# Optimization experiments

Hardware: AMD Instinct MI355X
Metric: run time of the kernel (lower is better)

Reference implementation:

```python
import jax, jax.numpy as jnp
import numpy as np

B, K = 2048, 256
ED = RD = HD = 256
AD = ED + RD          # action_dim = 512
IN = ED + HD + RD     # 768
NUM_E, NUM_R = 100000, 500
HUGE = jnp.float32(1e31)  # ops.HUGE_INT


def setup_inputs() -> dict:
    key = jax.random.key(0)
    ks = jax.random.split(key, 12)
    s = 0.05  # keep logits in a sane range
    E = jax.random.normal(ks[0], (B, ED), jnp.float32)
    H = jax.random.normal(ks[1], (B, HD), jnp.float32)
    Q = jax.random.normal(ks[2], (B, RD), jnp.float32)
    W1 = jax.random.normal(ks[3], (AD, IN), jnp.float32) * s
    b1 = jnp.zeros((AD,), jnp.float32)
    W2 = jax.random.normal(ks[4], (AD, AD), jnp.float32) * s
    b2 = jnp.zeros((AD,), jnp.float32)
    emb_r = jax.random.normal(ks[5], (NUM_R, RD), jnp.float32) * s
    emb_e = jax.random.normal(ks[6], (NUM_E, ED), jnp.float32) * s
    # binary action mask (variable-size action spaces, padded); col 0 always valid
    action_mask = (jax.random.uniform(ks[7], (B, K)) > 0.3).astype(jnp.float32)
    action_mask = action_mask.at[:, 0].set(1.0)
    r_space = jax.random.randint(ks[8], (B, K), 0, NUM_R)
    e_space = jax.random.randint(ks[9], (B, K), 0, NUM_E)
    return {"E": E, "H": H, "Q": Q, "W1": W1, "b1": b1, "W2": W2, "b2": b2,
            "emb_r": emb_r, "emb_e": emb_e, "action_mask": action_mask,
            "r_space": r_space, "e_space": e_space}


def reference(E, H, Q, W1, b1, W2, b2, emb_r, emb_e, action_mask, r_space, e_space):
    # state MLP: X = W2Dropout(W2(relu(W1(cat([E, H, Q])))))  (dropout = identity at eval)
    X = jnp.concatenate([E, H, Q], axis=-1)           # [B, IN]
    X = jax.nn.relu(X @ W1.T + b1)                    # [B, AD]
    X2 = X @ W2.T + b2                                # [B, AD]
    # gather action embeddings: A = cat([emb_r[r], emb_e[e]])  [B, K, AD]
    A = jnp.concatenate([emb_r[r_space], emb_e[e_space]], axis=-1)
    # masked softmax over action space
    scores = jnp.einsum('bkd,bd->bk', A, X2) - (1.0 - action_mask) * HUGE
    action_dist = jax.nn.softmax(scores, axis=-1)     # [B, K]
    entropy = -jnp.sum(action_dist * jnp.log(action_dist + 1e-20), axis=-1)  # [B]
    return action_dist, entropy
```

## Files before the change

kernel.cpp:

```cpp
#include <hip/hip_runtime.h>
#include <hip/hip_bf16.h>
#include <hip/hip_fp8.h>
#include <math.h>

#define B_   2048
#define K_   256
#define AD_  512
#define IN_  768
#define NR_  500
#define NRP_ 512
#define NE_  100000
#define PITCH 72

typedef __attribute__((ext_vector_type(8))) short short8;
typedef __attribute__((ext_vector_type(4))) float float4v;
typedef __attribute__((ext_vector_type(4))) float f32x4;

__device__ __forceinline__ unsigned short f2bf(float f) {
    unsigned int u = __float_as_uint(f);
    unsigned int r = u + 0x7FFF + ((u >> 16) & 1);
    return (unsigned short)(r >> 16);
}
__device__ __forceinline__ unsigned char f2fp8(float f) {
    __hip_fp8_e4m3 t(f);
    return (unsigned char)t.__x;
}
__device__ __forceinline__ float fp8tof(unsigned int byte) {
    __hip_fp8_e4m3 t; t.__x = (__hip_fp8_storage_t)byte; return (float)t;
}
__device__ __forceinline__ float dot4_fp8(unsigned int d, const float* x) {
    return fp8tof(d & 0xffu)         * x[0] + fp8tof((d >> 8) & 0xffu)  * x[1]
         + fp8tof((d >> 16) & 0xffu) * x[2] + fp8tof(d >> 24)           * x[3];
}
__device__ __forceinline__ short8 pack8(float4 a, float4 b) {
    short8 r;
    r[0] = (short)f2bf(a.x); r[1] = (short)f2bf(a.y);
    r[2] = (short)f2bf(a.z); r[3] = (short)f2bf(a.w);
    r[4] = (short)f2bf(b.x); r[5] = (short)f2bf(b.y);
    r[6] = (short)f2bf(b.z); r[7] = (short)f2bf(b.w);
    return r;
}

#define EE_N4 (NE_ * 256 / 4)
__device__ __forceinline__ void conv_range(
    const float* __restrict__ emb_e, unsigned char* __restrict__ emb_e8,
    int q0, int q1, int cb, int nb)
{
    const int stride = nb * 256;
    const f32x4* __restrict__ src = (const f32x4*)emb_e;
    uchar4* __restrict__ dst = (uchar4*)emb_e8;
    int i = q0 + cb * 256 + (int)threadIdx.x;
    for (; i + 3 * stride < q1; i += 4 * stride) {
        f32x4 v0 = __builtin_nontemporal_load(src + i);
        f32x4 v1 = __builtin_nontemporal_load(src + i + stride);
        f32x4 v2 = __builtin_nontemporal_load(src + i + 2 * stride);
        f32x4 v3 = __builtin_nontemporal_load(src + i + 3 * stride);
        uchar4 o0, o1, o2, o3;
        o0.x = f2fp8(v0[0]); o0.y = f2fp8(v0[1]); o0.z = f2fp8(v0[2]); o0.w = f2fp8(v0[3]);
        o1.x = f2fp8(v1[0]); o1.y = f2fp8(v1[1]); o1.z = f2fp8(v1[2]); o1.w = f2fp8(v1[3]);
        o2.x = f2fp8(v2[0]); o2.y = f2fp8(v2[1]); o2.z = f2fp8(v2[2]); o2.w = f2fp8(v2[3]);
        o3.x = f2fp8(v3[0]); o3.y = f2fp8(v3[1]); o3.z = f2fp8(v3[2]); o3.w = f2fp8(v3[3]);
        dst[i] = o0; dst[i + stride] = o1; dst[i + 2 * stride] = o2; dst[i + 3 * stride] = o3;
    }
    for (; i < q1; i += stride) {
        f32x4 v = __builtin_nontemporal_load(src + i);
        uchar4 o;
        o.x = f2fp8(v[0]); o.y = f2fp8(v[1]); o.z = f2fp8(v[2]); o.w = f2fp8(v[3]);
        dst[i] = o;
    }
}

__device__ __forceinline__ void br_compute(
    const float* __restrict__ emb_r, const float* __restrict__ b2,
    float* __restrict__ br, int blk)
{
    const int tid = threadIdx.x;
    const int rl = tid >> 3, sub = tid & 7;
    const int r = blk * 32 + rl;
    float acc = 0.0f;
    if (r < NR_) {
        const float4* er = (const float4*)&emb_r[(size_t)r * 256];
        const float4* bb = (const float4*)b2;
        #pragma unroll
        for (int i = 0; i < 8; ++i) {
            const float4 e = er[sub * 8 + i];
            const float4 c = bb[sub * 8 + i];
            acc += e.x * c.x + e.y * c.y + e.z * c.z + e.w * c.w;
        }
    }
    #pragma unroll
    for (int off = 4; off >= 1; off >>= 1) acc += __shfl_down(acc, off, 8);
    if (sub == 0) br[r] = (r < NR_) ? acc : 0.0f;
}

__device__ __forceinline__ void mfma_step(
    const ushort* __restrict__ Asb, const ushort* __restrict__ Bsb,
    int w, int q, int l16, float4v acc[4])
{
    #pragma unroll
    for (int kh = 0; kh < 64; kh += 32) {
        const short8 af = *(const short8*)&Asb[(w * 16 + l16) * PITCH + kh + q * 8];
        #pragma unroll
        for (int jn = 0; jn < 4; ++jn) {
            const short8 bfr = *(const short8*)&Bsb[(jn * 16 + l16) * PITCH + kh + q * 8];
            acc[jn] = __builtin_amdgcn_mfma_f32_16x16x32_bf16(af, bfr, acc[jn], 0, 0, 0);
        }
    }
}

__device__ __forceinline__ const float* ehq_ptr(
    const float* E, const float* H, const float* Q, int m, int k)
{
    return (k < 256) ? &E[(size_t)m * 256 + k]
         : (k < 512) ? &H[(size_t)m * 256 + (k - 256)]
                     : &Q[(size_t)m * 256 + (k - 512)];
}
__device__ __forceinline__ void ld_w2t(const float* __restrict__ W2, int col, int krow,
                                       short8& lo, short8& hi)
{
    float v[16];
    #pragma unroll
    for (int i = 0; i < 16; ++i) v[i] = W2[(size_t)(krow + i) * 512 + col];
    #pragma unroll
    for (int i = 0; i < 8; ++i) { lo[i] = (short)f2bf(v[i]); hi[i] = (short)f2bf(v[8 + i]); }
}
__device__ __forceinline__ void ld_embr(const float* __restrict__ emb_r, int row, int k,
                                        bool ok, short8& lo, short8& hi)
{
    if (ok) {
        const float4* p = (const float4*)&emb_r[(size_t)row * 256 + k];
        lo = pack8(p[0], p[1]); hi = pack8(p[2], p[3]);
    } else {
        #pragma unroll
        for (int i = 0; i < 8; ++i) { lo[i] = 0; hi[i] = 0; }
    }
}

__global__ __launch_bounds__(256) void k1_kernel(
    const float* __restrict__ E, const float* __restrict__ H,
    const float* __restrict__ Q, const float* __restrict__ W1,
    const float* __restrict__ b1, const float* __restrict__ emb_r,
    const float* __restrict__ b2, const float* __restrict__ W2,
    ushort* __restrict__ H1b, ushort* __restrict__ W2Rb, float* __restrict__ br,
    const float* __restrict__ emb_e, unsigned char* __restrict__ emb_e8,
    int q0, int q1, int nbconv)
{
    __shared__ ushort Asl[2][64 * PITCH];
    __shared__ ushort Bsl[2][64 * PITCH];
    const int tid = threadIdx.x;
    const int lane = tid & 63, w = tid >> 6;
    const int q = lane >> 4, l16 = lane & 15;
    const int lrow = tid >> 2, lcg = (tid & 3) * 16;

    if (blockIdx.x >= 8) {
        const int c = (int)(blockIdx.x - 8) * 32 + (int)blockIdx.y;
        if (c >= 80) { conv_range(emb_e, emb_e8, q0, q1, c - 80, nbconv); return; }
        if (c >= 64) { br_compute(emb_r, b2, br, c - 64); return; }
        const int n0 = (c & 7) * 64, m0 = (c >> 3) * 64;
        const int am = m0 + lrow;
        const bool aok = am < NR_;
        short8 pa0, pa1, pb0, pb1;
        ld_embr(emb_r, am, lcg, aok, pa0, pa1);
        ld_w2t(W2, n0 + lrow, lcg, pb0, pb1);
        *(short8*)&Asl[0][lrow * PITCH + lcg]     = pa0;
        *(short8*)&Asl[0][lrow * PITCH + lcg + 8] = pa1;
        *(short8*)&Bsl[0][lrow * PITCH + lcg]     = pb0;
        *(short8*)&Bsl[0][lrow * PITCH + lcg + 8] = pb1;
        float4v acc[4] = {};
        int buf = 0;
        __syncthreads();
        for (int k0 = 0; k0 < 256; k0 += 64) {
            if (k0 + 64 < 256) {
                ld_embr(emb_r, am, k0 + 64 + lcg, aok, pa0, pa1);
                ld_w2t(W2, n0 + lrow, k0 + 64 + lcg, pb0, pb1);
            }
            mfma_step(&Asl[buf][0], &Bsl[buf][0], w, q, l16, acc);
            if (k0 + 64 < 256) {
                *(short8*)&Asl[buf ^ 1][lrow * PITCH + lcg]     = pa0;
                *(short8*)&Asl[buf ^ 1][lrow * PITCH + lcg + 8] = pa1;
                *(short8*)&Bsl[buf ^ 1][lrow * PITCH + lcg]     = pb0;
                *(short8*)&Bsl[buf ^ 1][lrow * PITCH + lcg + 8] = pb1;
                __syncthreads();
                buf ^= 1;
            }
        }
        #pragma unroll
        for (int jn = 0; jn < 4; ++jn) {
            const int n = n0 + jn * 16 + l16;
            #pragma unroll
            for (int r = 0; r < 4; ++r) {
                const int m = m0 + w * 16 + q * 4 + r;
                W2Rb[(size_t)m * 512 + n] = f2bf(acc[jn][r]);
            }
        }
        return;
    }

    const int n0 = blockIdx.x * 64, m0 = blockIdx.y * 64;
    const int am = m0 + lrow;
    const float* w1p = &W1[(size_t)(n0 + lrow) * 768 + lcg];

    short8 pa0, pa1, pb0, pb1;
    {
        const float4* ap = (const float4*)ehq_ptr(E, H, Q, am, lcg);
        pa0 = pack8(ap[0], ap[1]); pa1 = pack8(ap[2], ap[3]);
        const float4* bp = (const float4*)w1p;
        pb0 = pack8(bp[0], bp[1]); pb1 = pack8(bp[2], bp[3]);
    }
    *(short8*)&Asl[0][lrow * PITCH + lcg]     = pa0;
    *(short8*)&Asl[0][lrow * PITCH + lcg + 8] = pa1;
    *(short8*)&Bsl[0][lrow * PITCH + lcg]     = pb0;
    *(short8*)&Bsl[0][lrow * PITCH + lcg + 8] = pb1;
    float4v acc[4] = {};
    int buf = 0;
    __syncthreads();
    for (int k0 = 0; k0 < 768; k0 += 64) {
        if (k0 + 64 < 768) {
            const float4* ap = (const float4*)ehq_ptr(E, H, Q, am, k0 + 64 + lcg);
            pa0 = pack8(ap[0], ap[1]); pa1 = pack8(ap[2], ap[3]);
            const float4* bp = (const float4*)(w1p + k0 + 64);
            pb0 = pack8(bp[0], bp[1]); pb1 = pack8(bp[2], bp[3]);
        }
        mfma_step(&Asl[buf][0], &Bsl[buf][0], w, q, l16, acc);
        if (k0 + 64 < 768) {
            *(short8*)&Asl[buf ^ 1][lrow * PITCH + lcg]     = pa0;
            *(short8*)&Asl[buf ^ 1][lrow * PITCH + lcg + 8] = pa1;
            *(short8*)&Bsl[buf ^ 1][lrow * PITCH + lcg]     = pb0;
            *(short8*)&Bsl[buf ^ 1][lrow * PITCH + lcg + 8] = pb1;
            __syncthreads();
            buf ^= 1;
        }
    }
    #pragma unroll
    for (int jn = 0; jn < 4; ++jn) {
        const int n = n0 + jn * 16 + l16;
        const float bn = b1[n];
        #pragma unroll
        for (int r = 0; r < 4; ++r) {
            const int m = m0 + w * 16 + q * 4 + r;
            H1b[(size_t)m * AD_ + n] = f2bf(fmaxf(acc[jn][r] + bn, 0.0f));
        }
    }
}

__global__ __launch_bounds__(256) void k2_kernel(
    const ushort* __restrict__ H1b, const float* __restrict__ W2,
    const ushort* __restrict__ W2Rb, const float* __restrict__ b2,
    const float* __restrict__ br, float* __restrict__ X2e, float* __restrict__ Rt,
    const float* __restrict__ emb_e, unsigned char* __restrict__ emb_e8,
    int q0, int q1, int nbconv)
{
    __shared__ ushort Asl[2][64 * PITCH];
    __shared__ ushort Bsl[2][64 * PITCH];
    if (blockIdx.x >= 12) {
        conv_range(emb_e, emb_e8, q0, q1,
                   (int)(blockIdx.x - 12) * 32 + (int)blockIdx.y, nbconv);
        return;
    }
    const int tid = threadIdx.x;
    const int lane = tid & 63, w = tid >> 6;
    const int q = lane >> 4, l16 = lane & 15;
    const int lrow = tid >> 2, lcg = (tid & 3) * 16;
    const bool isR = blockIdx.x >= 4;
    const int n0 = isR ? (int)(blockIdx.x - 4) * 64 : (int)blockIdx.x * 64;
    const int m0 = blockIdx.y * 64;

    const ushort* aptr  = &H1b[(size_t)(m0 + lrow) * 512 + lcg];
    const ushort* bptrR = &W2Rb[(size_t)(n0 + lrow) * 512 + lcg];
    const float*  bptrW = &W2[(size_t)(256 + n0 + lrow) * 512 + lcg];

    short8 pa0, pa1, pb0, pb1;
    pa0 = *(const short8*)aptr; pa1 = *(const short8*)(aptr + 8);
    if (isR) { pb0 = *(const short8*)bptrR; pb1 = *(const short8*)(bptrR + 8); }
    else {
        const float4* bp = (const float4*)bptrW;
        pb0 = pack8(bp[0], bp[1]); pb1 = pack8(bp[2], bp[3]);
    }
    *(short8*)&Asl[0][lrow * PITCH + lcg]     = pa0;
    *(short8*)&Asl[0][lrow * PITCH + lcg + 8] = pa1;
    *(short8*)&Bsl[0][lrow * PITCH + lcg]     = pb0;
    *(short8*)&Bsl[0][lrow * PITCH + lcg + 8] = pb1;
    float4v acc[4] = {};
    int buf = 0;
    __syncthreads();
    for (int k0 = 0; k0 < 512; k0 += 64) {
        if (k0 + 64 < 512) {
            pa0 = *(const short8*)(aptr + k0 + 64);
            pa1 = *(const short8*)(aptr + k0 + 64 + 8);
            if (isR) {
                pb0 = *(const short8*)(bptrR + k0 + 64);
                pb1 = *(const short8*)(bptrR + k0 + 64 + 8);
            } else {
                const float4* bp = (const float4*)(bptrW + k0 + 64);
                pb0 = pack8(bp[0], bp[1]); pb1 = pack8(bp[2], bp[3]);
            }
        }
        mfma_step(&Asl[buf][0], &Bsl[buf][0], w, q, l16, acc);
        if (k0 + 64 < 512) {
            *(short8*)&Asl[buf ^ 1][lrow * PITCH + lcg]     = pa0;
            *(short8*)&Asl[buf ^ 1][lrow * PITCH + lcg + 8] = pa1;
            *(short8*)&Bsl[buf ^ 1][lrow * PITCH + lcg]     = pb0;
            *(short8*)&Bsl[buf ^ 1][lrow * PITCH + lcg + 8] = pb1;
            __syncthreads();
            buf ^= 1;
        }
    }
    #pragma unroll
    for (int jn = 0; jn < 4; ++jn) {
        const int n = n0 + jn * 16 + l16;
        const float bn = isR ? br[n] : b2[256 + n];
        #pragma unroll
        for (int r = 0; r < 4; ++r) {
            const int m = m0 + w * 16 + q * 4 + r;
            const float cv = acc[jn][r] + bn;
            if (isR) Rt[(size_t)m * 512 + n] = cv;
            else     X2e[(size_t)m * 256 + n] = cv;
        }
    }
}

__global__ __launch_bounds__(256) void scores_kernel(
    const float* __restrict__ X2e, const float* __restrict__ R,
    const unsigned char* __restrict__ emb_e8, const float* __restrict__ mask,
    const int* __restrict__ r_space, const int* __restrict__ e_space,
    float* __restrict__ dist, float* __restrict__ entropy)
{
    const int b = blockIdx.x;
    const int tid = threadIdx.x;
    const int lane = tid & 63, wid = tid >> 6;
    const int l16 = lane & 15, q4 = lane >> 4;

    __shared__ int   s_e[K_];
    __shared__ float s_dot[K_];
    __shared__ float s_red[12];

    const int   e_mine = e_space[b * K_ + tid];
    const int   r_mine = r_space[b * K_ + tid];
    const float mk     = mask[b * K_ + tid];
    s_e[tid] = (mk != 0.0f) ? e_mine : 0;
    const float bias   = R[(size_t)b * NRP_ + r_mine] - (1.0f - mk) * 1e31f;
    float x[16];
    #pragma unroll
    for (int i = 0; i < 4; ++i) {
        const float4 xv = *(const float4*)&X2e[(size_t)b * 256 + l16 * 16 + i * 4];
        x[i * 4 + 0] = xv.x; x[i * 4 + 1] = xv.y;
        x[i * 4 + 2] = xv.z; x[i * 4 + 3] = xv.w;
    }
    __syncthreads();

    const int kbase = wid * 64;
    #pragma unroll
    for (int it = 0; it < 2; ++it) {
        uint4 wv[8];
        #pragma unroll
        for (int u = 0; u < 8; ++u) {
            const int row = kbase + it * 32 + u * 4 + q4;
            const int e = s_e[row];
            wv[u] = *(const uint4*)&emb_e8[(size_t)e * 256 + l16 * 16];
        }
        float p[8];
        #pragma unroll
        for (int u = 0; u < 8; ++u) {
            p[u] = dot4_fp8(wv[u].x, &x[0]) + dot4_fp8(wv[u].y, &x[4])
                 + dot4_fp8(wv[u].z, &x[8]) + dot4_fp8(wv[u].w, &x[12]);
        }
        #pragma unroll
        for (int off = 8; off >= 1; off >>= 1) {
            #pragma unroll
            for (int u = 0; u < 8; ++u) p[u] += __shfl_down(p[u], off, 16);
        }
        if (l16 == 0) {
            #pragma unroll
            for (int u = 0; u < 8; ++u) s_dot[kbase + it * 32 + u * 4 + q4] = p[u];
        }
    }
    __syncthreads();

    const float v = s_dot[tid] + bias;

    float m = v;
    #pragma unroll
    for (int off = 32; off >= 1; off >>= 1) m = fmaxf(m, __shfl_down(m, off));
    if (lane == 0) s_red[wid] = m;
    __syncthreads();
    if (tid == 0)
        s_red[8] = fmaxf(fmaxf(s_red[0], s_red[1]), fmaxf(s_red[2], s_red[3]));
    __syncthreads();
    const float bmax = s_red[8];

    const float ev = __expf(v - bmax);
    float s = ev;
    float t = ev * (v - bmax);
    #pragma unroll
    for (int off = 32; off >= 1; off >>= 1) {
        s += __shfl_down(s, off);
        t += __shfl_down(t, off);
    }
    if (lane == 0) { s_red[wid] = s; s_red[4 + wid] = t; }
    __syncthreads();
    if (tid == 0) {
        s_red[9]  = s_red[0] + s_red[1] + s_red[2] + s_red[3];
        s_red[10] = s_red[4] + s_red[5] + s_red[6] + s_red[7];
    }
    __syncthreads();
    const float ssum = s_red[9];

    dist[(size_t)b * K_ + tid] = ev / ssum;
    if (tid == 0)
        entropy[b] = logf(ssum) - s_red[10] / ssum;
}

extern "C" void kernel_launch(void* const* d_in, const int* in_sizes, int n_in,
                              void* d_out, int out_size, void* d_ws, size_t ws_size,
                              hipStream_t stream) {
    const float* E     = (const float*)d_in[0];
    const float* H     = (const float*)d_in[1];
    const float* Q     = (const float*)d_in[2];
    const float* W1    = (const float*)d_in[3];
    const float* b1    = (const float*)d_in[4];
    const float* W2    = (const float*)d_in[5];
    const float* b2    = (const float*)d_in[6];
    const float* emb_r = (const float*)d_in[7];
    const float* emb_e = (const float*)d_in[8];
    const float* mask  = (const float*)d_in[9];
    const int* r_space = (const int*)d_in[10];
    const int* e_space = (const int*)d_in[11];

    float* out_dist = (float*)d_out;
    float* out_ent  = out_dist + (size_t)B_ * K_;

    char* ws = (char*)d_ws;
    unsigned char* emb_e8 = (unsigned char*)ws; ws += (size_t)NE_ * 256;
    ushort* H1b  = (ushort*)ws;  ws += (size_t)B_ * AD_ * 2;
    ushort* W2Rb = (ushort*)ws;  ws += (size_t)512 * 512 * 2;
    float*  X2e  = (float*)ws;   ws += (size_t)B_ * 256 * 4;
    float*  Rt   = (float*)ws;   ws += (size_t)B_ * NRP_ * 4;
    float*  br   = (float*)ws;   ws += (size_t)NRP_ * 4;

    const int Q1V = 3712000;

    dim3 g(16, 32);
    k1_kernel<<<g, 256, 0, stream>>>(E, H, Q, W1, b1, emb_r, b2, W2,
                                     H1b, W2Rb, br, emb_e, emb_e8, 0, Q1V, 176);
    k2_kernel<<<g, 256, 0, stream>>>(H1b, W2, W2Rb, b2, br, X2e, Rt,
                                     emb_e, emb_e8, Q1V, EE_N4, 128);
    scores_kernel<<<B_, 256, 0, stream>>>(X2e, Rt, emb_e8, mask,
                                          r_space, e_space, out_dist, out_ent);
}
```

Baseline: 214.6 us.

## Pre-convert GEMM inputs to bf16 in a prep kernel and widen score gather batch

Adds a prep kernel that converts the concatenated E/H/Q input, W1 and the entity half of W2 to bf16 once. The two GEMM kernels then load bf16 tiles directly through a shared templated tile routine, which removes the fp32 loads and per-tile packing inside the MFMA loops. The scores kernel now issues all 16 gathered emb_e8 row loads per thread at once instead of two batches of 8, to expose more memory-level parallelism. The cost is an extra kernel launch, an extra round trip of the small tensors through memory, and higher register use in the scores kernel.

```diff
diff --git a/kernel.cpp b/kernel.cpp
--- a/kernel.cpp
+++ b/kernel.cpp
@@ -39,6 +39,39 @@
     r[4] = (short)f2bf(b.x); r[5] = (short)f2bf(b.y);
     r[6] = (short)f2bf(b.z); r[7] = (short)f2bf(b.w);
     return r;
+}
+
+#define X_N4   (B_ * IN_ / 4)
+#define W1_N4  (AD_ * IN_ / 4)
+#define W2E_N4 (256 * AD_ / 4)
+#define PREPS_TOTAL (X_N4 + W1_N4 + W2E_N4)
+__global__ __launch_bounds__(256) void prep_small_kernel(
+    const float* __restrict__ E, const float* __restrict__ H,
+    const float* __restrict__ Q, const float* __restrict__ W1,
+    const float* __restrict__ W2,
+    ushort* __restrict__ Xb, ushort* __restrict__ W1b, ushort* __restrict__ W2eb)
+{
+    int t = blockIdx.x * 256 + threadIdx.x;
+    const float* src; ushort* dst; int off;
+    if (t < X_N4) {
+        const int base = t * 4;
+        const int row = base / IN_, col = base % IN_;
+        src = (col < 256) ? &E[row * 256 + col]
+            : (col < 512) ? &H[row * 256 + col - 256]
+                          : &Q[row * 256 + col - 512];
+        const float4 v = *(const float4*)src;
+        ushort4 o;
+        o.x = f2bf(v.x); o.y = f2bf(v.y); o.z = f2bf(v.z); o.w = f2bf(v.w);
+        *(ushort4*)&Xb[base] = o;
+        return;
+    }
+    t -= X_N4;
+    if (t < W1_N4) { src = W1;                dst = W1b;  off = t; }
+    else           { src = W2 + 256 * AD_;    dst = W2eb; off = t - W1_N4; }
+    const float4 v = *(const float4*)&src[off * 4];
+    ushort4 o;
+    o.x = f2bf(v.x); o.y = f2bf(v.y); o.z = f2bf(v.z); o.w = f2bf(v.w);
+    *(ushort4*)&dst[off * 4] = o;
 }
 
 #define EE_N4 (NE_ * 256 / 4)
@@ -90,7 +123,7 @@
     }
     #pragma unroll
     for (int off = 4; off >= 1; off >>= 1) acc += __shfl_down(acc, off, 8);
-    if (sub == 0) br[r] = (r < NR_) ? acc : 0.0f;
+    if (sub == 0 && r < NRP_) br[r] = (r < NR_) ? acc : 0.0f;
 }
 
 __device__ __forceinline__ void mfma_step(
@@ -108,13 +141,66 @@
     }
 }
 
-__device__ __forceinline__ const float* ehq_ptr(
-    const float* E, const float* H, const float* Q, int m, int k)
-{
-    return (k < 256) ? &E[(size_t)m * 256 + k]
-         : (k < 512) ? &H[(size_t)m * 256 + (k - 256)]
-                     : &Q[(size_t)m * 256 + (k - 512)];
-}
+template<int K, bool RELU, bool OUT_BF16>
+__device__ __forceinline__ void gemm_tile(
+    const ushort* __restrict__ A, const ushort* __restrict__ Bw,
+    const float* __restrict__ bias, ushort* __restrict__ outb,
+    float* __restrict__ outf, const int ostride,
+    const int n0, const int m0, ushort* __restrict__ As, ushort* __restrict__ Bs)
+{
+    const int tid = threadIdx.x;
+    const int lane = tid & 63, w = tid >> 6;
+    const int lrow = tid >> 2, lcg = (tid & 3) * 16;
+    const int q = lane >> 4, l16 = lane & 15;
+
+    const ushort* aptr = &A[(size_t)(m0 + lrow) * K + lcg];
+    const ushort* bptr = &Bw[(size_t)(n0 + lrow) * K + lcg];
+
+    short8 ra0 = *(const short8*)aptr;
+    short8 ra1 = *(const short8*)(aptr + 8);
+    short8 rb0 = *(const short8*)bptr;
+    short8 rb1 = *(const short8*)(bptr + 8);
+    *(short8*)&As[lrow * PITCH + lcg]     = ra0;
+    *(short8*)&As[lrow * PITCH + lcg + 8] = ra1;
+    *(short8*)&Bs[lrow * PITCH + lcg]     = rb0;
+    *(short8*)&Bs[lrow * PITCH + lcg + 8] = rb1;
+
+    float4v acc[4] = {};
+    int buf = 0;
+    __syncthreads();
+    for (int k0 = 0; k0 < K; k0 += 64) {
+        if (k0 + 64 < K) {
+            ra0 = *(const short8*)(aptr + k0 + 64);
+            ra1 = *(const short8*)(aptr + k0 + 64 + 8);
+            rb0 = *(const short8*)(bptr + k0 + 64);
+            rb1 = *(const short8*)(bptr + k0 + 64 + 8);
+        }
+        mfma_step(As + buf * 64 * PITCH, Bs + buf * 64 * PITCH, w, q, l16, acc);
+        if (k0 + 64 < K) {
+            const int nb = (buf ^ 1) * 64 * PITCH;
+            *(short8*)&As[nb + lrow * PITCH + lcg]     = ra0;
+            *(short8*)&As[nb + lrow * PITCH + lcg + 8] = ra1;
+            *(short8*)&Bs[nb + lrow * PITCH + lcg]     = rb0;
+            *(short8*)&Bs[nb + lrow * PITCH + lcg + 8] = rb1;
+            __syncthreads();
+            buf ^= 1;
+        }
+    }
+    #pragma unroll
+    for (int jn = 0; jn < 4; ++jn) {
+        const int n = n0 + jn * 16 + l16;
+        const float bn = bias[n];
+        #pragma unroll
+        for (int r = 0; r < 4; ++r) {
+            const int m = m0 + w * 16 + q * 4 + r;
+            float c = acc[jn][r] + bn;
+            if (RELU) c = fmaxf(c, 0.0f);
+            if (OUT_BF16) outb[(size_t)m * ostride + n] = f2bf(c);
+            else          outf[(size_t)m * ostride + n] = c;
+        }
+    }
+}
+
 __device__ __forceinline__ void ld_w2t(const float* __restrict__ W2, int col, int krow,
                                        short8& lo, short8& hi)
 {
@@ -135,187 +221,99 @@
         for (int i = 0; i < 8; ++i) { lo[i] = 0; hi[i] = 0; }
     }
 }
+__device__ __forceinline__ void w2r_tile(
+    const float* __restrict__ emb_r, const float* __restrict__ W2,
+    ushort* __restrict__ W2Rb, const int n0, const int m0,
+    ushort* __restrict__ As, ushort* __restrict__ Bs)
+{
+    const int tid = threadIdx.x;
+    const int lane = tid & 63, w = tid >> 6;
+    const int q = lane >> 4, l16 = lane & 15;
+    const int lrow = tid >> 2, lcg = (tid & 3) * 16;
+    const int am = m0 + lrow;
+    const bool aok = am < NR_;
+    short8 pa0, pa1, pb0, pb1;
+    ld_embr(emb_r, am, lcg, aok, pa0, pa1);
+    ld_w2t(W2, n0 + lrow, lcg, pb0, pb1);
+    *(short8*)&As[lrow * PITCH + lcg]     = pa0;
+    *(short8*)&As[lrow * PITCH + lcg + 8] = pa1;
+    *(short8*)&Bs[lrow * PITCH + lcg]     = pb0;
+    *(short8*)&Bs[lrow * PITCH + lcg + 8] = pb1;
+    float4v acc[4] = {};
+    int buf = 0;
+    __syncthreads();
+    for (int k0 = 0; k0 < 256; k0 += 64) {
+        if (k0 + 64 < 256) {
+            ld_embr(emb_r, am, k0 + 64 + lcg, aok, pa0, pa1);
+            ld_w2t(W2, n0 + lrow, k0 + 64 + lcg, pb0, pb1);
+        }
+        mfma_step(As + buf * 64 * PITCH, Bs + buf * 64 * PITCH, w, q, l16, acc);
+        if (k0 + 64 < 256) {
+            const int nb = (buf ^ 1) * 64 * PITCH;
+            *(short8*)&As[nb + lrow * PITCH + lcg]     = pa0;
+            *(short8*)&As[nb + lrow * PITCH + lcg + 8] = pa1;
+            *(short8*)&Bs[nb + lrow * PITCH + lcg]     = pb0;
+            *(short8*)&Bs[nb + lrow * PITCH + lcg + 8] = pb1;
+            __syncthreads();
+            buf ^= 1;
+        }
+    }
+    #pragma unroll
+    for (int jn = 0; jn < 4; ++jn) {
+        const int n = n0 + jn * 16 + l16;
+        #pragma unroll
+        for (int r = 0; r < 4; ++r) {
+            const int m = m0 + w * 16 + q * 4 + r;
+            W2Rb[(size_t)m * 512 + n] = f2bf(acc[jn][r]);
+        }
+    }
+}
 
 __global__ __launch_bounds__(256) void k1_kernel(
-    const float* __restrict__ E, const float* __restrict__ H,
-    const float* __restrict__ Q, const float* __restrict__ W1,
+    const ushort* __restrict__ Xb, const ushort* __restrict__ W1b,
     const float* __restrict__ b1, const float* __restrict__ emb_r,
     const float* __restrict__ b2, const float* __restrict__ W2,
     ushort* __restrict__ H1b, ushort* __restrict__ W2Rb, float* __restrict__ br,
     const float* __restrict__ emb_e, unsigned char* __restrict__ emb_e8,
-    int q0, int q1, int nbconv)
+    int q0, int q1)
 {
     __shared__ ushort Asl[2][64 * PITCH];
     __shared__ ushort Bsl[2][64 * PITCH];
-    const int tid = threadIdx.x;
-    const int lane = tid & 63, w = tid >> 6;
-    const int q = lane >> 4, l16 = lane & 15;
-    const int lrow = tid >> 2, lcg = (tid & 3) * 16;
-
     if (blockIdx.x >= 8) {
         const int c = (int)(blockIdx.x - 8) * 32 + (int)blockIdx.y;
-        if (c >= 80) { conv_range(emb_e, emb_e8, q0, q1, c - 80, nbconv); return; }
-        if (c >= 64) { br_compute(emb_r, b2, br, c - 64); return; }
-        const int n0 = (c & 7) * 64, m0 = (c >> 3) * 64;
-        const int am = m0 + lrow;
-        const bool aok = am < NR_;
-        short8 pa0, pa1, pb0, pb1;
-        ld_embr(emb_r, am, lcg, aok, pa0, pa1);
-        ld_w2t(W2, n0 + lrow, lcg, pb0, pb1);
-        *(short8*)&Asl[0][lrow * PITCH + lcg]     = pa0;
-        *(short8*)&Asl[0][lrow * PITCH + lcg + 8] = pa1;
-        *(short8*)&Bsl[0][lrow * PITCH + lcg]     = pb0;
-        *(short8*)&Bsl[0][lrow * PITCH + lcg + 8] = pb1;
-        float4v acc[4] = {};
-        int buf = 0;
-        __syncthreads();
-        for (int k0 = 0; k0 < 256; k0 += 64) {
-            if (k0 + 64 < 256) {
-                ld_embr(emb_r, am, k0 + 64 + lcg, aok, pa0, pa1);
-                ld_w2t(W2, n0 + lrow, k0 + 64 + lcg, pb0, pb1);
-            }
-            mfma_step(&Asl[buf][0], &Bsl[buf][0], w, q, l16, acc);
-            if (k0 + 64 < 256) {
-                *(short8*)&Asl[buf ^ 1][lrow * PITCH + lcg]     = pa0;
-                *(short8*)&Asl[buf ^ 1][lrow * PITCH + lcg + 8] = pa1;
-                *(short8*)&Bsl[buf ^ 1][lrow * PITCH + lcg]     = pb0;
-                *(short8*)&Bsl[buf ^ 1][lrow * PITCH + lcg + 8] = pb1;
-                __syncthreads();
-                buf ^= 1;
-            }
-        }
-        #pragma unroll
-        for (int jn = 0; jn < 4; ++jn) {
-            const int n = n0 + jn * 16 + l16;
-            #pragma unroll
-            for (int r = 0; r < 4; ++r) {
-                const int m = m0 + w * 16 + q * 4 + r;
-                W2Rb[(size_t)m * 512 + n] = f2bf(acc[jn][r]);
-            }
-        }
+        if (c >= 80)      conv_range(emb_e, emb_e8, q0, q1, c - 80, 176);
+        else if (c >= 64) br_compute(emb_r, b2, br, c - 64);
+        else              w2r_tile(emb_r, W2, W2Rb, (c & 7) * 64, (c >> 3) * 64,
+                                   &Asl[0][0], &Bsl[0][0]);
         return;
     }
-
-    const int n0 = blockIdx.x * 64, m0 = blockIdx.y * 64;
-    const int am = m0 + lrow;
-    const float* w1p = &W1[(size_t)(n0 + lrow) * 768 + lcg];
-
-    short8 pa0, pa1, pb0, pb1;
-    {
-        const float4* ap = (const float4*)ehq_ptr(E, H, Q, am, lcg);
-        pa0 = pack8(ap[0], ap[1]); pa1 = pack8(ap[2], ap[3]);
-        const float4* bp = (const float4*)w1p;
-        pb0 = pack8(bp[0], bp[1]); pb1 = pack8(bp[2], bp[3]);
-    }
-    *(short8*)&Asl[0][lrow * PITCH + lcg]     = pa0;
-    *(short8*)&Asl[0][lrow * PITCH + lcg + 8] = pa1;
-    *(short8*)&Bsl[0][lrow * PITCH + lcg]     = pb0;
-    *(short8*)&Bsl[0][lrow * PITCH + lcg + 8] = pb1;
-    float4v acc[4] = {};
-    int buf = 0;
-    __syncthreads();
-    for (int k0 = 0; k0 < 768; k0 += 64) {
-        if (k0 + 64 < 768) {
-            const float4* ap = (const float4*)ehq_ptr(E, H, Q, am, k0 + 64 + lcg);
-            pa0 = pack8(ap[0], ap[1]); pa1 = pack8(ap[2], ap[3]);
-            const float4* bp = (const float4*)(w1p + k0 + 64);
-            pb0 = pack8(bp[0], bp[1]); pb1 = pack8(bp[2], bp[3]);
-        }
-        mfma_step(&Asl[buf][0], &Bsl[buf][0], w, q, l16, acc);
-        if (k0 + 64 < 768) {
-            *(short8*)&Asl[buf ^ 1][lrow * PITCH + lcg]     = pa0;
-            *(short8*)&Asl[buf ^ 1][lrow * PITCH + lcg + 8] = pa1;
-            *(short8*)&Bsl[buf ^ 1][lrow * PITCH + lcg]     = pb0;
-            *(short8*)&Bsl[buf ^ 1][lrow * PITCH + lcg + 8] = pb1;
-            __syncthreads();
-            buf ^= 1;
-        }
-    }
-    #pragma unroll
-    for (int jn = 0; jn < 4; ++jn) {
-        const int n = n0 + jn * 16 + l16;
-        const float bn = b1[n];
-        #pragma unroll
-        for (int r = 0; r < 4; ++r) {
-            const int m = m0 + w * 16 + q * 4 + r;
-            H1b[(size_t)m * AD_ + n] = f2bf(fmaxf(acc[jn][r] + bn, 0.0f));
-        }
-    }
+    gemm_tile<IN_, true, true>(Xb, W1b, b1, H1b, nullptr, AD_,
+                               (int)blockIdx.x * 64, (int)blockIdx.y * 64,
+                               &Asl[0][0], &Bsl[0][0]);
 }
 
 __global__ __launch_bounds__(256) void k2_kernel(
-    const ushort* __restrict__ H1b, const float* __restrict__ W2,
-    const ushort* __restrict__ W2Rb, const float* __restrict__ b2,
+    const ushort* __restrict__ H1b, const ushort* __restrict__ W2eb,
+    const ushort* __restrict__ W2Rb, const float* __restrict__ b2e,
     const float* __restrict__ br, float* __restrict__ X2e, float* __restrict__ Rt,
     const float* __restrict__ emb_e, unsigned char* __restrict__ emb_e8,
-    int q0, int q1, int nbconv)
+    int q0, int q1)
 {
     __shared__ ushort Asl[2][64 * PITCH];
     __shared__ ushort Bsl[2][64 * PITCH];
     if (blockIdx.x >= 12) {
         conv_range(emb_e, emb_e8, q0, q1,
-                   (int)(blockIdx.x - 12) * 32 + (int)blockIdx.y, nbconv);
+                   (int)(blockIdx.x - 12) * 32 + (int)blockIdx.y, 128);
         return;
     }
-    const int tid = threadIdx.x;
-    const int lane = tid & 63, w = tid >> 6;
-    const int q = lane >> 4, l16 = lane & 15;
-    const int lrow = tid >> 2, lcg = (tid & 3) * 16;
-    const bool isR = blockIdx.x >= 4;
-    const int n0 = isR ? (int)(blockIdx.x - 4) * 64 : (int)blockIdx.x * 64;
-    const int m0 = blockIdx.y * 64;
-
-    const ushort* aptr  = &H1b[(size_t)(m0 + lrow) * 512 + lcg];
-    const ushort* bptrR = &W2Rb[(size_t)(n0 + lrow) * 512 + lcg];
-    const float*  bptrW = &W2[(size_t)(256 + n0 + lrow) * 512 + lcg];
-
-    short8 pa0, pa1, pb0, pb1;
-    pa0 = *(const short8*)aptr; pa1 = *(const short8*)(aptr + 8);
-    if (isR) { pb0 = *(const short8*)bptrR; pb1 = *(const short8*)(bptrR + 8); }
-    else {
-        const float4* bp = (const float4*)bptrW;
-        pb0 = pack8(bp[0], bp[1]); pb1 = pack8(bp[2], bp[3]);
-    }
-    *(short8*)&Asl[0][lrow * PITCH + lcg]     = pa0;
-    *(short8*)&Asl[0][lrow * PITCH + lcg + 8] = pa1;
-    *(short8*)&Bsl[0][lrow * PITCH + lcg]     = pb0;
-    *(short8*)&Bsl[0][lrow * PITCH + lcg + 8] = pb1;
-    float4v acc[4] = {};
-    int buf = 0;
-    __syncthreads();
-    for (int k0 = 0; k0 < 512; k0 += 64) {
-        if (k0 + 64 < 512) {
-            pa0 = *(const short8*)(aptr + k0 + 64);
-            pa1 = *(const short8*)(aptr + k0 + 64 + 8);
-            if (isR) {
-                pb0 = *(const short8*)(bptrR + k0 + 64);
-                pb1 = *(const short8*)(bptrR + k0 + 64 + 8);
-            } else {
-                const float4* bp = (const float4*)(bptrW + k0 + 64);
-                pb0 = pack8(bp[0], bp[1]); pb1 = pack8(bp[2], bp[3]);
-            }
-        }
-        mfma_step(&Asl[buf][0], &Bsl[buf][0], w, q, l16, acc);
-        if (k0 + 64 < 512) {
-            *(short8*)&Asl[buf ^ 1][lrow * PITCH + lcg]     = pa0;
-            *(short8*)&Asl[buf ^ 1][lrow * PITCH + lcg + 8] = pa1;
-            *(short8*)&Bsl[buf ^ 1][lrow * PITCH + lcg]     = pb0;
-            *(short8*)&Bsl[buf ^ 1][lrow * PITCH + lcg + 8] = pb1;
-            __syncthreads();
-            buf ^= 1;
-        }
-    }
-    #pragma unroll
-    for (int jn = 0; jn < 4; ++jn) {
-        const int n = n0 + jn * 16 + l16;
-        const float bn = isR ? br[n] : b2[256 + n];
-        #pragma unroll
-        for (int r = 0; r < 4; ++r) {
-            const int m = m0 + w * 16 + q * 4 + r;
-            const float cv = acc[jn][r] + bn;
-            if (isR) Rt[(size_t)m * 512 + n] = cv;
-            else     X2e[(size_t)m * 256 + n] = cv;
-        }
+    if (blockIdx.x < 4) {
+        gemm_tile<AD_, false, false>(H1b, W2eb, b2e, nullptr, X2e, 256,
+                                     (int)blockIdx.x * 64, (int)blockIdx.y * 64,
+                                     &Asl[0][0], &Bsl[0][0]);
+    } else {
+        gemm_tile<AD_, false, false>(H1b, W2Rb, br, nullptr, Rt, NRP_,
+                                     (int)(blockIdx.x - 4) * 64, (int)blockIdx.y * 64,
+                                     &Asl[0][0], &Bsl[0][0]);
     }
 }
 
@@ -349,30 +347,26 @@
     __syncthreads();
 
     const int kbase = wid * 64;
-    #pragma unroll
-    for (int it = 0; it < 2; ++it) {
-        uint4 wv[8];
-        #pragma unroll
-        for (int u = 0; u < 8; ++u) {
-            const int row = kbase + it * 32 + u * 4 + q4;
-            const int e = s_e[row];
-            wv[u] = *(const uint4*)&emb_e8[(size_t)e * 256 + l16 * 16];
-        }
-        float p[8];
-        #pragma unroll
-        for (int u = 0; u < 8; ++u) {
-            p[u] = dot4_fp8(wv[u].x, &x[0]) + dot4_fp8(wv[u].y, &x[4])
-                 + dot4_fp8(wv[u].z, &x[8]) + dot4_fp8(wv[u].w, &x[12]);
-        }
-        #pragma unroll
-        for (int off = 8; off >= 1; off >>= 1) {
-            #pragma unroll
-            for (int u = 0; u < 8; ++u) p[u] += __shfl_down(p[u], off, 16);
-        }
-        if (l16 == 0) {
-            #pragma unroll
-            for (int u = 0; u < 8; ++u) s_dot[kbase + it * 32 + u * 4 + q4] = p[u];
-        }
+    uint4 wv[16];
+    #pragma unroll
+    for (int u = 0; u < 16; ++u) {
+        const int row = kbase + u * 4 + q4;
+        wv[u] = *(const uint4*)&emb_e8[(size_t)s_e[row] * 256 + l16 * 16];
+    }
+    float p[16];
+    #pragma unroll
+    for (int u = 0; u < 16; ++u) {
+        p[u] = dot4_fp8(wv[u].x, &x[0]) + dot4_fp8(wv[u].y, &x[4])
+             + dot4_fp8(wv[u].z, &x[8]) + dot4_fp8(wv[u].w, &x[12]);
+    }
+    #pragma unroll
+    for (int off = 8; off >= 1; off >>= 1) {
+        #pragma unroll
+        for (int u = 0; u < 16; ++u) p[u] += __shfl_down(p[u], off, 16);
+    }
+    if (l16 == 0) {
+        #pragma unroll
+        for (int u = 0; u < 16; ++u) s_dot[kbase + u * 4 + q4] = p[u];
     }
     __syncthreads();
 
@@ -431,6 +425,9 @@
 
     char* ws = (char*)d_ws;
     unsigned char* emb_e8 = (unsigned char*)ws; ws += (size_t)NE_ * 256;
+    ushort* Xb   = (ushort*)ws;  ws += (size_t)B_ * IN_ * 2;
+    ushort* W1b  = (ushort*)ws;  ws += (size_t)AD_ * IN_ * 2;
+    ushort* W2eb = (ushort*)ws;  ws += (size_t)256 * AD_ * 2;
     ushort* H1b  = (ushort*)ws;  ws += (size_t)B_ * AD_ * 2;
     ushort* W2Rb = (ushort*)ws;  ws += (size_t)512 * 512 * 2;
     float*  X2e  = (float*)ws;   ws += (size_t)B_ * 256 * 4;
@@ -439,11 +436,14 @@
 
     const int Q1V = 3712000;
 
+    prep_small_kernel<<<PREPS_TOTAL / 256, 256, 0, stream>>>(
+        E, H, Q, W1, W2, Xb, W1b, W2eb);
+
     dim3 g(16, 32);
-    k1_kernel<<<g, 256, 0, stream>>>(E, H, Q, W1, b1, emb_r, b2, W2,
-                                     H1b, W2Rb, br, emb_e, emb_e8, 0, Q1V, 176);
-    k2_kernel<<<g, 256, 0, stream>>>(H1b, W2, W2Rb, b2, br, X2e, Rt,
-                                     emb_e, emb_e8, Q1V, EE_N4, 128);
+    k1_kernel<<<g, 256, 0, stream>>>(Xb, W1b, b1, emb_r, b2, W2,
+                                     H1b, W2Rb, br, emb_e, emb_e8, 0, Q1V);
+    k2_kernel<<<g, 256, 0, stream>>>(H1b, W2eb, W2Rb, b2 + 256, br, X2e, Rt,
+                                     emb_e, emb_e8, Q1V, EE_N4);
     scores_kernel<<<B_, 256, 0, stream>>>(X2e, Rt, emb_e8, mask,
                                           r_space, e_space, out_dist, out_ent);
 }
```

Measured after the change: 221.0 us. 1.03x slower.
